# Kernel optimization log

Measured on AMD Instinct MI355X. Metric: run time of the kernel, lower is better.

Reference implementation:

```python
import jax, jax.numpy as jnp
import numpy as np
from functools import partial

H = 51  # hidden size hard-coded in the module


def _lstm_cell(x, h, c, W_ih, b_ih, W_hh, b_hh):
    # PyTorch LSTMCell gate order: i, f, g, o stacked along dim 0 of W (4H rows)
    gates = x @ W_ih.T + b_ih + h @ W_hh.T + b_hh  # [B, 4H]
    i, f, g, o = jnp.split(gates, 4, axis=-1)
    i = jax.nn.sigmoid(i)
    f = jax.nn.sigmoid(f)
    g = jnp.tanh(g)
    o = jax.nn.sigmoid(o)
    c_new = f * c + i * g
    h_new = o * jnp.tanh(c_new)
    return h_new, c_new


def setup_inputs() -> dict:
    key = jax.random.key(0)
    ks = jax.random.split(key, 11)
    B, T = 2048, 512
    bound = 1.0 / np.sqrt(H)  # torch LSTMCell/Linear default init: U(-1/sqrt(H), 1/sqrt(H))
    u = lambda k, shape: jax.random.uniform(k, shape, jnp.float32, -bound, bound)
    return {
        "x": jax.random.normal(ks[0], (B, T), dtype=jnp.float32),
        "future": 0,
        "W_ih1": u(ks[1], (4 * H, 1)),
        "b_ih1": u(ks[2], (4 * H,)),
        "W_hh1": u(ks[3], (4 * H, H)),
        "b_hh1": u(ks[4], (4 * H,)),
        "W_ih2": u(ks[5], (4 * H, H)),
        "b_ih2": u(ks[6], (4 * H,)),
        "W_hh2": u(ks[7], (4 * H, H)),
        "b_hh2": u(ks[8], (4 * H,)),
        "fc_w": u(ks[9], (1, H)),
        "fc_b": u(ks[10], (1,)),
    }


def reference(x, future, W_ih1, b_ih1, W_hh1, b_hh1,
              W_ih2, b_ih2, W_hh2, b_hh2, fc_w, fc_b):
    B = x.shape[0]
    z = jnp.zeros((B, H), dtype=x.dtype)

    def cell_stack(x_t, carry):
        h1, c1, h2, c2 = carry
        h1, c1 = _lstm_cell(x_t, h1, c1, W_ih1, b_ih1, W_hh1, b_hh1)
        h2, c2 = _lstm_cell(h1, h2, c2, W_ih2, b_ih2, W_hh2, b_hh2)
        out = h2 @ fc_w.T + fc_b  # [B, 1]
        return (h1, c1, h2, c2), out

    def step(carry, x_t):
        return cell_stack(x_t, carry)

    xs = jnp.swapaxes(x, 0, 1)[:, :, None]  # [T, B, 1]
    carry, outs = jax.lax.scan(step, (z, z, z, z), xs)  # outs: [T, B, 1]
    outputs = jnp.swapaxes(outs[:, :, 0], 0, 1)  # [B, T]

    if future > 0:
        last = outs[-1]  # [B, 1]

        def fstep(c, _):
            inner, out = c
            inner, out = cell_stack(out, inner)
            return (inner, out), out

        _, fouts = jax.lax.scan(fstep, (carry, last), None, length=future)
        outputs = jnp.concatenate([outputs, jnp.swapaxes(fouts[:, :, 0], 0, 1)], axis=1)

    return outputs
```

## Files before the change

kernel.cpp:

```cpp
#include <hip/hip_runtime.h>

#define HID   51
#define T_LEN 512
#define BT    8
#define NTH   832

#define X_OFF   0
#define OUT_OFF 4128
#define H1_OFF  8256
#define H2_OFF  9280

typedef _Float16 h8 __attribute__((ext_vector_type(8)));
typedef float    f4 __attribute__((ext_vector_type(4)));

__device__ __forceinline__ float fast_rcp(float x) { return __builtin_amdgcn_rcpf(x); }
__device__ __forceinline__ float sigm(float x) { return fast_rcp(1.0f + __expf(-x)); }
__device__ __forceinline__ float tanh_f(float x) {
    x = fminf(15.0f, fmaxf(-15.0f, x));
    float e = __expf(2.0f * x);
    return (e - 1.0f) * fast_rcp(e + 1.0f);
}
__device__ __forceinline__ float tanh_nc(float x) {
    float e = __expf(2.0f * x);
    return (e - 1.0f) * fast_rcp(e + 1.0f);
}

__device__ __forceinline__ float dpp_ror8(float v) {
    int t = __builtin_amdgcn_update_dpp(0, __float_as_int(v), 0x128, 0xf, 0xf, true);
    return __int_as_float(t);
}

__device__ __forceinline__ h8 cvt_frag1(const float* p) {
    float4 a = *(const float4*)p;
    float4 b = *(const float4*)(p + 4);
    h8 h;
    h[0] = (_Float16)a.x; h[1] = (_Float16)a.y; h[2] = (_Float16)a.z; h[3] = (_Float16)a.w;
    h[4] = (_Float16)b.x; h[5] = (_Float16)b.y; h[6] = (_Float16)b.z; h[7] = (_Float16)b.w;
    return h;
}

__device__ __forceinline__ float gate_update(const float G[4], float& c) {
    float iv = sigm(G[0]), fv = sigm(G[1]), gv = tanh_nc(G[2]), ov = sigm(G[3]);
    c = fv * c + iv * gv;
    return ov * tanh_f(c);
}

#define MFMA16(A, B, C) __builtin_amdgcn_mfma_f32_16x16x32_f16((A), (B), (C), 0, 0, 0)

__global__ __launch_bounds__(NTH)
void lstm_seq_kernel(const float* __restrict__ x,
                     const float* __restrict__ W_ih1, const float* __restrict__ b_ih1,
                     const float* __restrict__ W_hh1, const float* __restrict__ b_hh1,
                     const float* __restrict__ W_ih2, const float* __restrict__ b_ih2,
                     const float* __restrict__ W_hh2, const float* __restrict__ b_hh2,
                     const float* __restrict__ fc_w,  const float* __restrict__ fc_b,
                     float* __restrict__ out)
{
    __shared__ __align__(16) float sb[13312];

    const int tid   = threadIdx.x;
    const int b0    = blockIdx.x * BT;
    const int w     = tid >> 6;
    const int lane  = tid & 63;
    const int row16 = lane & 15;
    const int q4    = lane >> 4;
    const int col   = row16;

    h8 a1f[2];
    h8 a2f[4];

    for (int i = tid; i < 208 * 64; i += NTH) {
        int rp = i >> 6, k = i & 63;
        int j = rp >> 2, g = rp & 3;
        float v = 0.0f;
        if (j < HID) {
            if (k < HID)       v = W_hh1[(g * HID + j) * HID + k];
            else if (k == HID) v = W_ih1[g * HID + j];
        }
        sb[i] = v;
    }
    __syncthreads();
    #pragma unroll
    for (int kt = 0; kt < 2; ++kt)
        a1f[kt] = cvt_frag1(sb + (w * 16 + row16) * 64 + kt * 32 + q4 * 8);
    __syncthreads();

    for (int i = tid; i < 208 * 64; i += NTH) {
        int rp = i >> 6, k = i & 63;
        int j = rp >> 2, g = rp & 3;
        sb[i] = (j < HID && k < HID) ? W_ih2[(g * HID + j) * HID + k] : 0.0f;
    }
    __syncthreads();
    #pragma unroll
    for (int kt = 0; kt < 2; ++kt)
        a2f[kt] = cvt_frag1(sb + (w * 16 + row16) * 64 + kt * 32 + q4 * 8);
    __syncthreads();

    for (int i = tid; i < 208 * 64; i += NTH) {
        int rp = i >> 6, k = i & 63;
        int j = rp >> 2, g = rp & 3;
        float v = 0.0f;
        if (k < HID) {
            if (j < HID)        v = W_hh2[(g * HID + j) * HID + k];
            else if (rp == 204) v = fc_w[k];
        }
        sb[i] = v;
    }
    __syncthreads();
    #pragma unroll
    for (int kt = 0; kt < 2; ++kt)
        a2f[kt + 2] = cvt_frag1(sb + (w * 16 + row16) * 64 + kt * 32 + q4 * 8);
    __syncthreads();

    const int jq = 4 * w + q4;
    f4 bi1, bi2;
    #pragma unroll
    for (int g = 0; g < 4; ++g) {
        bi1[g] = (jq < HID) ? (b_ih1[g * HID + jq] + b_hh1[g * HID + jq]) : 0.f;
        bi2[g] = (jq < HID) ? (b_ih2[g * HID + jq] + b_hh2[g * HID + jq]) : 0.f;
    }
    const bool lay1 = (col < 8);
    const int  bsel = col & 7;
    const bool val  = (jq < HID);
    const int offh  = (lay1 ? H1_OFF : H2_OFF) * 2
                    + (jq >> 5) * 512 + ((((jq & 31) >> 3) << 4) + bsel) * 8 + (jq & 7);
    const bool xw = (jq == HID) && lay1;

    float* xl   = sb + X_OFF;
    float* outl = sb + OUT_OFF;
    for (int i = tid; i < BT * 516; i += NTH) {
        int b = i / 516, t = i - 516 * b;
        xl[i] = (t < T_LEN) ? x[(size_t)(b0 + b) * T_LEN + t] : 0.0f;
    }
    for (int i = tid; i < 2048; i += NTH) sb[H1_OFF + i] = 0.0f;

    float c = 0.f;
    const float fcb = fc_b[0];
    const bool outlane = (w == 12) && (q4 == 3) && (col < 8);
    const float* xq  = xl + bsel * 516;
    const float* rA0 = sb + H1_OFF + lane * 4;
    const float* rB0 = sb + H2_OFF + lane * 4;
    _Float16* hwp = (_Float16*)sb + offh;
    __syncthreads();

    if (lay1) {
        if (val) {
            float xv = xq[0];
            float G[4];
            #pragma unroll
            for (int g = 0; g < 4; ++g)
                G[g] = bi1[g] + W_ih1[g * HID + jq] * xv;
            float hv = gate_update(G, c);
            hwp[0] = (_Float16)hv;
        } else if (xw) {
            hwp[0] = (_Float16)xq[1];
        }
    }
    __syncthreads();

    auto body = [&](int i, int p) {
        const float* rA = rA0 + p * 512;
        const float* rB = rB0 + p * 512;
        h8 bh0 = *(const h8*)(rA);       h8 bh1 = *(const h8*)(rA + 256);
        h8 ch2 = *(const h8*)(rB);       h8 ch3 = *(const h8*)(rB + 256);

        if (xw) hwp[(p ^ 1) * 1024] = (_Float16)xq[i + 2];

        f4 s = bi1;
        s = MFMA16(a1f[0], bh0, s);
        s = MFMA16(a1f[1], bh1, s);
        f4 u = bi2;
        u = MFMA16(a2f[0], bh0, u);
        u = MFMA16(a2f[1], bh1, u);
        u = MFMA16(a2f[2], ch2, u);
        u = MFMA16(a2f[3], ch3, u);

        float fcv = u[0];
        float G[4];
        #pragma unroll
        for (int g = 0; g < 4; ++g) {
            float ur = dpp_ror8(u[g]);
            G[g] = lay1 ? s[g] : ur;
        }
        float hv = gate_update(G, c);
        if (val) hwp[(p ^ 1) * 1024] = (_Float16)hv;
        if (outlane && i >= 1) outl[col * 516 + (i - 1)] = fcb + fcv;
        __syncthreads();
    };
    for (int i = 0; i < T_LEN; i += 2) {
        body(i, 0);
        body(i + 1, 1);
    }
    body(T_LEN, 0);

    for (int i = tid; i < BT * T_LEN; i += NTH) {
        int b = i >> 9, tt = i & (T_LEN - 1);
        out[(size_t)(b0 + b) * T_LEN + tt] = outl[b * 516 + tt];
    }
}

extern "C" void kernel_launch(void* const* d_in, const int* in_sizes, int n_in,
                              void* d_out, int out_size, void* d_ws, size_t ws_size,
                              hipStream_t stream) {
    const float* x      = (const float*)d_in[0];
    const float* W_ih1  = (const float*)d_in[2];
    const float* b_ih1v = (const float*)d_in[3];
    const float* W_hh1  = (const float*)d_in[4];
    const float* b_hh1v = (const float*)d_in[5];
    const float* W_ih2  = (const float*)d_in[6];
    const float* b_ih2v = (const float*)d_in[7];
    const float* W_hh2  = (const float*)d_in[8];
    const float* b_hh2v = (const float*)d_in[9];
    const float* fc_w   = (const float*)d_in[10];
    const float* fc_b   = (const float*)d_in[11];
    float* out = (float*)d_out;

    dim3 grid(2048 / BT);
    dim3 block(NTH);
    lstm_seq_kernel<<<grid, block, 0, stream>>>(x, W_ih1, b_ih1v, W_hh1, b_hh1v,
                                                W_ih2, b_ih2v, W_hh2, b_hh2v,
                                                fc_w, fc_b, out);
}
```

Before: 377.0 us.

## Pack layer-1 and layer-2 hidden states into one shared MFMA B fragment

Stores h1 and h2 side by side as the two halves of a single 16-column fp16 tile, so each step loads one B fragment pair instead of two. Layer-2 input and recurrent products are computed as separate MFMAs over the combined tile and merged via a DPP rotate plus add. This reduces LDS reads and shared-memory footprint per step in the latency-bound recurrence. It adds a few VALU adds per gate and changes which lanes hold the fc output.

```diff
diff --git a/kernel.cpp b/kernel.cpp
--- a/kernel.cpp
+++ b/kernel.cpp
@@ -7,8 +7,7 @@
 
 #define X_OFF   0
 #define OUT_OFF 4128
-#define H1_OFF  8256
-#define H2_OFF  9280
+#define H_OFF   8256
 
 typedef _Float16 h8 __attribute__((ext_vector_type(8)));
 typedef float    f4 __attribute__((ext_vector_type(4)));
@@ -67,7 +66,8 @@
     const int col   = row16;
 
     h8 a1f[2];
-    h8 a2f[4];
+    h8 a2if[2];
+    h8 a2hf[2];
 
     for (int i = tid; i < 208 * 64; i += NTH) {
         int rp = i >> 6, k = i & 63;
@@ -93,7 +93,7 @@
     __syncthreads();
     #pragma unroll
     for (int kt = 0; kt < 2; ++kt)
-        a2f[kt] = cvt_frag1(sb + (w * 16 + row16) * 64 + kt * 32 + q4 * 8);
+        a2if[kt] = cvt_frag1(sb + (w * 16 + row16) * 64 + kt * 32 + q4 * 8);
     __syncthreads();
 
     for (int i = tid; i < 208 * 64; i += NTH) {
@@ -109,7 +109,7 @@
     __syncthreads();
     #pragma unroll
     for (int kt = 0; kt < 2; ++kt)
-        a2f[kt + 2] = cvt_frag1(sb + (w * 16 + row16) * 64 + kt * 32 + q4 * 8);
+        a2hf[kt] = cvt_frag1(sb + (w * 16 + row16) * 64 + kt * 32 + q4 * 8);
     __syncthreads();
 
     const int jq = 4 * w + q4;
@@ -122,8 +122,9 @@
     const bool lay1 = (col < 8);
     const int  bsel = col & 7;
     const bool val  = (jq < HID);
-    const int offh  = (lay1 ? H1_OFF : H2_OFF) * 2
-                    + (jq >> 5) * 512 + ((((jq & 31) >> 3) << 4) + bsel) * 8 + (jq & 7);
+    const int  cpos = lay1 ? bsel : (8 + bsel);
+    const int  offh = H_OFF * 2
+                    + (jq >> 5) * 512 + ((((jq & 31) >> 3) << 4) + cpos) * 8 + (jq & 7);
     const bool xw = (jq == HID) && lay1;
 
     float* xl   = sb + X_OFF;
@@ -132,14 +133,13 @@
         int b = i / 516, t = i - 516 * b;
         xl[i] = (t < T_LEN) ? x[(size_t)(b0 + b) * T_LEN + t] : 0.0f;
     }
-    for (int i = tid; i < 2048; i += NTH) sb[H1_OFF + i] = 0.0f;
+    for (int i = tid; i < 1024; i += NTH) sb[H_OFF + i] = 0.0f;
 
     float c = 0.f;
     const float fcb = fc_b[0];
-    const bool outlane = (w == 12) && (q4 == 3) && (col < 8);
+    const bool outlane = (w == 12) && (q4 == 3) && (col >= 8);
     const float* xq  = xl + bsel * 516;
-    const float* rA0 = sb + H1_OFF + lane * 4;
-    const float* rB0 = sb + H2_OFF + lane * 4;
+    const float* rA0 = sb + H_OFF + lane * 4;
     _Float16* hwp = (_Float16*)sb + offh;
     __syncthreads();
 
@@ -160,31 +160,30 @@
 
     auto body = [&](int i, int p) {
         const float* rA = rA0 + p * 512;
-        const float* rB = rB0 + p * 512;
-        h8 bh0 = *(const h8*)(rA);       h8 bh1 = *(const h8*)(rA + 256);
-        h8 ch2 = *(const h8*)(rB);       h8 ch3 = *(const h8*)(rB + 256);
+        h8 bb0 = *(const h8*)(rA);       h8 bb1 = *(const h8*)(rA + 256);
 
         if (xw) hwp[(p ^ 1) * 1024] = (_Float16)xq[i + 2];
 
         f4 s = bi1;
-        s = MFMA16(a1f[0], bh0, s);
-        s = MFMA16(a1f[1], bh1, s);
-        f4 u = bi2;
-        u = MFMA16(a2f[0], bh0, u);
-        u = MFMA16(a2f[1], bh1, u);
-        u = MFMA16(a2f[2], ch2, u);
-        u = MFMA16(a2f[3], ch3, u);
-
-        float fcv = u[0];
+        s = MFMA16(a1f[0], bb0, s);
+        s = MFMA16(a1f[1], bb1, s);
+        f4 u = {0.f, 0.f, 0.f, 0.f};
+        u = MFMA16(a2if[0], bb0, u);
+        u = MFMA16(a2if[1], bb1, u);
+        f4 v = bi2;
+        v = MFMA16(a2hf[0], bb0, v);
+        v = MFMA16(a2hf[1], bb1, v);
+
+        float fcv = v[0];
         float G[4];
         #pragma unroll
         for (int g = 0; g < 4; ++g) {
-            float ur = dpp_ror8(u[g]);
-            G[g] = lay1 ? s[g] : ur;
+            float ug = dpp_ror8(u[g]) + v[g];
+            G[g] = lay1 ? s[g] : ug;
         }
         float hv = gate_update(G, c);
         if (val) hwp[(p ^ 1) * 1024] = (_Float16)hv;
-        if (outlane && i >= 1) outl[col * 516 + (i - 1)] = fcb + fcv;
+        if (outlane && i >= 1) outl[(col - 8) * 516 + (i - 1)] = fcb + fcv;
         __syncthreads();
     };
     for (int i = 0; i < T_LEN; i += 2) {
```

New measurement: 378.0 us. About the same (+0.3%).
